# Kernel optimization log

Hardware: AMD Instinct MI355X
Metric: run time of the kernel (lower is better)

The kernel has to match this reference:

```python
import jax, jax.numpy as jnp
import numpy as np

B, N_Q, N_KV, D, H = 2, 2048, 2048, 512, 8
HD = D // H
NEG = -10000.0
LN_EPS = 1e-5


def setup_inputs() -> dict:
    key = jax.random.key(0)
    ks = jax.random.split(key, 8)
    s = 1.0 / np.sqrt(D)
    return {
        "query": jax.random.normal(ks[0], (B, N_Q, D), jnp.float32),
        "key_value": jax.random.normal(ks[1], (B, N_KV, D), jnp.float32),
        "Wq": jax.random.normal(ks[2], (D, D), jnp.float32) * s,
        "bq": jnp.zeros((D,), jnp.float32),
        "Wk": jax.random.normal(ks[3], (D, D), jnp.float32) * s,
        "bk": jnp.zeros((D,), jnp.float32),
        "Wv": jax.random.normal(ks[4], (D, D), jnp.float32) * s,
        "bv": jnp.zeros((D,), jnp.float32),
        "ln_gamma": jnp.ones((D,), jnp.float32),
        "ln_beta": jnp.zeros((D,), jnp.float32),
    }


def reference(query, key_value, Wq, bq, Wk, bk, Wv, bv, ln_gamma, ln_beta):
    # combined sequence [B, S, D], S = N_q + N_kv
    combined = jnp.concatenate([query, key_value], axis=1)
    Bt, S, _ = combined.shape
    n_q = query.shape[1]

    def heads(x, W, b):
        return (x @ W + b).reshape(Bt, S, H, HD)

    q = heads(combined, Wq, bq)  # [B,S,H,hd]
    k = heads(combined, Wk, bk)
    v = heads(combined, Wv, bv)

    scores = jnp.einsum("bqhd,bkhd->bhqk", q, k) / jnp.sqrt(
        jnp.asarray(HD, q.dtype)
    )
    # additive mask: -10000 on key columns < N_q for every query row
    key_mask = jnp.where(jnp.arange(S) < n_q, jnp.asarray(NEG, q.dtype), 0.0)
    probs = jax.nn.softmax(scores + key_mask[None, None, None, :], axis=-1)
    ctx = jnp.einsum("bhqk,bkhd->bqhd", probs, v).reshape(Bt, S, D)

    attended_q = ctx[:, :n_q, :]  # [B, N_q, D]
    resid = query + attended_q  # dropout is identity in eval
    mu = jnp.mean(resid, axis=-1, keepdims=True)
    var = jnp.var(resid, axis=-1, keepdims=True)
    out = (resid - mu) / jnp.sqrt(var + LN_EPS) * ln_gamma + ln_beta
    return out
```

## Files before the change

kernel.cpp:

```cpp
#include <hip/hip_runtime.h>
#include <stdint.h>

#define B_     2
#define NQ     2048
#define NKV    2048
#define D_     512
#define H_     8
#define HD     64
#define MROWS  4096
#define NSPLIT 4
#define SKEYS  (NKV / NSPLIT)

typedef unsigned short u16;
typedef __attribute__((ext_vector_type(4))) unsigned short u16x4;
typedef __attribute__((ext_vector_type(8))) unsigned short u16x8;
typedef __attribute__((ext_vector_type(8))) __bf16 bf16x8;
typedef __attribute__((ext_vector_type(4))) float f32x4;

__device__ __forceinline__ u16 f2bf(float f) {
  union { float f; unsigned int u; } v; v.f = f;
  unsigned int u = v.u;
  unsigned int r = (u + 0x7FFFu + ((u >> 16) & 1u)) >> 16;
  return (u16)r;
}
__device__ __forceinline__ float bf2f(u16 b) {
  union { unsigned int u; float f; } v; v.u = ((unsigned int)b) << 16;
  return v.f;
}
__device__ __forceinline__ unsigned cvtpk(float a, float b) {
  unsigned r;
  asm("v_cvt_pk_bf16_f32 %0, %1, %2" : "=v"(r) : "v"(a), "v"(b));
  return r;
}

__device__ __forceinline__ f32x4 mfma16(u16x8 a, u16x8 b, f32x4 c) {
  return __builtin_amdgcn_mfma_f32_16x16x32_bf16(
      __builtin_bit_cast(bf16x8, a), __builtin_bit_cast(bf16x8, b), c, 0, 0, 0);
}

#define QSCL 0.18033688011112042f

__global__ __launch_bounds__(256) void cast_act_kernel(
    const float* __restrict__ q, const float* __restrict__ kv,
    u16* __restrict__ qb, u16* __restrict__ kvb) {
  int i = blockIdx.x * 256 + threadIdx.x;
  float4 a = ((const float4*)q)[i];
  float4 b = ((const float4*)kv)[i];
  u16x4 ua = { f2bf(a.x), f2bf(a.y), f2bf(a.z), f2bf(a.w) };
  u16x4 ub = { f2bf(b.x), f2bf(b.y), f2bf(b.z), f2bf(b.w) };
  ((u16x4*)qb)[i]  = ua;
  ((u16x4*)kvb)[i] = ub;
}

__global__ __launch_bounds__(256) void wtrans_kernel(
    const float* __restrict__ Wq, const float* __restrict__ Wk,
    const float* __restrict__ Wv,
    u16* __restrict__ wqt, u16* __restrict__ wkt, u16* __restrict__ wvt) {
  __shared__ float tile[32][33];
  int bx = blockIdx.x;
  int which = bx >> 8;
  int t = bx & 255;
  int tr = t >> 4, tc = t & 15;
  const float* W = (which == 0) ? Wq : (which == 1) ? Wk : Wv;
  u16* WT = (which == 0) ? wqt : (which == 1) ? wkt : wvt;

  int tx = threadIdx.x & 31, ty = threadIdx.x >> 5;
#pragma unroll
  for (int i = 0; i < 4; ++i)
    tile[ty + 8 * i][tx] = W[(size_t)(tr * 32 + ty + 8 * i) * D_ + tc * 32 + tx];
  __syncthreads();
#pragma unroll
  for (int i = 0; i < 4; ++i)
    WT[(size_t)(tc * 32 + ty + 8 * i) * D_ + tr * 32 + tx] =
        f2bf(tile[tx][ty + 8 * i]);
}

__global__ __launch_bounds__(256, 3) void gemm_qkv(
    const u16* __restrict__ qb, const u16* __restrict__ kvb,
    const u16* __restrict__ wqt, const u16* __restrict__ wkt,
    const u16* __restrict__ wvt,
    const float* __restrict__ bq, const float* __restrict__ bk,
    const float* __restrict__ bv,
    u16* __restrict__ Qp, u16* __restrict__ Kp, u16* __restrict__ VpT) {
  int lane = threadIdx.x & 63, w = threadIdx.x >> 6;
  int wr = w >> 1, wc = w & 1;
  int cl = lane & 15, g = lane >> 4;
  int cb = blockIdx.y;
  int which = cb >> 2;
  int row0 = blockIdx.x * 64, col0 = (cb & 3) * 128;

  const u16* A   = (which == 0) ? qb : kvb;
  const u16* WT  = (which == 0) ? wqt : (which == 1) ? wkt : wvt;
  const float* bias = (which == 0) ? bq : (which == 1) ? bk : bv;
  u16* Out = (which == 0) ? Qp : (which == 1) ? Kp : VpT;
  float oscale = (which == 0) ? QSCL : 1.0f;

  f32x4 acc[2][4] = {};
  const u16* Abase = A  + (size_t)(row0 + wr * 32 + cl) * D_ + g * 8;
  const u16* Bbase = WT + (size_t)(col0 + wc * 64 + cl) * D_ + g * 8;

  u16x8 afA[2], bfA[4], afB[2], bfB[4];
#pragma unroll
  for (int i = 0; i < 2; ++i) afA[i] = *(const u16x8*)(Abase + (size_t)i * 16 * D_);
#pragma unroll
  for (int j = 0; j < 4; ++j) bfA[j] = *(const u16x8*)(Bbase + (size_t)j * 16 * D_);

#pragma unroll
  for (int kk = 0; kk < 16; ++kk) {
    const u16x8* ca = (kk & 1) ? afB : afA;
    const u16x8* cw = (kk & 1) ? bfB : bfA;
    u16x8* na = (kk & 1) ? afA : afB;
    u16x8* nw = (kk & 1) ? bfA : bfB;
    if (kk < 15) {
      int k0 = kk * 32 + 32;
#pragma unroll
      for (int i = 0; i < 2; ++i) na[i] = *(const u16x8*)(Abase + (size_t)i * 16 * D_ + k0);
#pragma unroll
      for (int j = 0; j < 4; ++j) nw[j] = *(const u16x8*)(Bbase + (size_t)j * 16 * D_ + k0);
    }
#pragma unroll
    for (int i = 0; i < 2; ++i)
#pragma unroll
      for (int j = 0; j < 4; ++j)
        acc[i][j] = mfma16(ca[i], cw[j], acc[i][j]);
  }

#pragma unroll
  for (int j = 0; j < 4; ++j) {
    int col = col0 + wc * 64 + j * 16 + cl;
    float bv2 = bias[col];
#pragma unroll
    for (int i = 0; i < 2; ++i) {
      int rowb = row0 + wr * 32 + i * 16 + g * 4;
      if (which != 2) {
#pragma unroll
        for (int r = 0; r < 4; ++r)
          Out[(size_t)(rowb + r) * D_ + col] = f2bf((acc[i][j][r] + bv2) * oscale);
      } else {
        int b_ = rowb >> 11, key = rowb & (NKV - 1);
        u16x4 pk = { f2bf(acc[i][j][0] + bv2), f2bf(acc[i][j][1] + bv2),
                     f2bf(acc[i][j][2] + bv2), f2bf(acc[i][j][3] + bv2) };
        *(u16x4*)(Out + (size_t)b_ * (D_ * NKV) + (size_t)col * NKV + key) = pk;
      }
    }
  }
}

__global__ __launch_bounds__(64, 2) void attn_kernel(
    const u16* __restrict__ Q, const u16* __restrict__ K,
    const u16* __restrict__ VpT, u16* __restrict__ opart,
    float* __restrict__ ml) {
  __shared__ union __align__(16) {
    u16 p[64][66];
    unsigned t[64][33];
  } sm;

  int lane = threadIdx.x;
  int cl = lane & 15, g = lane >> 4;
  int q0 = blockIdx.x * 64;
  int s  = blockIdx.y;
  int bh = blockIdx.z;
  int b = bh >> 3, h = bh & 7;

  u16x8 qf[4][2];
  {
    const u16* Qb = Q + ((size_t)(b * NQ + q0 + cl)) * D_ + h * HD + g * 8;
#pragma unroll
    for (int f = 0; f < 4; ++f)
#pragma unroll
      for (int kk = 0; kk < 2; ++kk)
        qf[f][kk] = *(const u16x8*)(Qb + (size_t)f * 16 * D_ + kk * 32);
  }

  const u16* kptr[4];
  const u16* vptr[4];
#pragma unroll
  for (int kf_ = 0; kf_ < 4; ++kf_)
    kptr[kf_] = K + ((size_t)b * NKV + s * SKEYS + kf_ * 16 + cl) * D_ + h * HD + g * 8;
#pragma unroll
  for (int j = 0; j < 4; ++j)
    vptr[j] = VpT + (size_t)b * (D_ * NKV) + (size_t)(h * HD + j * 16 + cl) * NKV
                  + s * SKEYS + g * 8;

  f32x4 o[4][4] = {};
  float lsum[4] = { 0.f, 0.f, 0.f, 0.f };

  const int NT = SKEYS / 64;

  for (int t = 0; t < NT; ++t) {
    u16x8 kf[4][2];
#pragma unroll
    for (int kf_ = 0; kf_ < 4; ++kf_)
#pragma unroll
      for (int kk = 0; kk < 2; ++kk)
        kf[kf_][kk] = *(const u16x8*)(kptr[kf_] + kk * 32);

    f32x4 sa[4][4] = {};
    __builtin_amdgcn_s_setprio(1);
#pragma unroll
    for (int kk = 0; kk < 2; ++kk)
#pragma unroll
      for (int kf_ = 0; kf_ < 4; ++kf_)
#pragma unroll
        for (int f = 0; f < 4; ++f)
          sa[kf_][f] = mfma16(kf[kf_][kk], qf[f][kk], sa[kf_][f]);
    __builtin_amdgcn_s_setprio(0);

    u16x8 vf[4][2];
#pragma unroll
    for (int j = 0; j < 4; ++j)
#pragma unroll
      for (int kk = 0; kk < 2; ++kk)
        vf[j][kk] = *(const u16x8*)(vptr[j] + kk * 32);

#pragma unroll
    for (int f = 0; f < 4; ++f) {
      float ps = 0.f;
#pragma unroll
      for (int kf_ = 0; kf_ < 4; ++kf_)
#pragma unroll
        for (int r = 0; r < 4; ++r) {
          float p = exp2f(sa[kf_][f][r]);
          sa[kf_][f][r] = p;
          ps += p;
        }
      lsum[f] += ps;
    }

#pragma unroll
    for (int f = 0; f < 4; ++f)
#pragma unroll
      for (int kf_ = 0; kf_ < 4; ++kf_) {
        unsigned lo = cvtpk(sa[kf_][f][0], sa[kf_][f][1]);
        unsigned hi = cvtpk(sa[kf_][f][2], sa[kf_][f][3]);
        unsigned* P32 = (unsigned*)&sm.p[f * 16 + cl][kf_ * 16 + g * 4];
        P32[0] = lo;
        P32[1] = hi;
      }

#pragma unroll
    for (int kk = 0; kk < 2; ++kk) {
      __builtin_amdgcn_s_setprio(1);
#pragma unroll
      for (int f = 0; f < 4; ++f) {
        u16x8 pa = *(const u16x8*)&sm.p[f * 16 + cl][kk * 32 + g * 8];
#pragma unroll
        for (int j = 0; j < 4; ++j)
          o[f][j] = mfma16(vf[j][kk], pa, o[f][j]);
      }
      __builtin_amdgcn_s_setprio(0);
    }

#pragma unroll
    for (int kf_ = 0; kf_ < 4; ++kf_) kptr[kf_] += 64 * D_;
#pragma unroll
    for (int j = 0; j < 4; ++j) vptr[j] += 64;
  }

#pragma unroll
  for (int f = 0; f < 4; ++f) {
    lsum[f] += __shfl_xor(lsum[f], 16, 64);
    lsum[f] += __shfl_xor(lsum[f], 32, 64);
  }

#pragma unroll
  for (int f = 0; f < 4; ++f)
#pragma unroll
    for (int j = 0; j < 4; ++j) {
      int row = f * 16 + cl;
      sm.t[row][j * 8 + g * 2 + 0] = cvtpk(o[f][j][0], o[f][j][1]);
      sm.t[row][j * 8 + g * 2 + 1] = cvtpk(o[f][j][2], o[f][j][3]);
    }
  if (g == 0) {
#pragma unroll
    for (int f = 0; f < 4; ++f) {
      size_t mi = ((size_t)(bh * NSPLIT + s) * NQ + q0 + f * 16 + cl) * 2;
      ml[mi]     = 0.f;
      ml[mi + 1] = lsum[f];
    }
  }
  __syncthreads();
  {
    int row = lane;
    u16* op = opart + (size_t)(bh * NSPLIT + s) * NQ * HD + (size_t)(q0 + row) * HD;
#pragma unroll
    for (int i = 0; i < 8; ++i) {
      uint4 v;
      v.x = sm.t[row][i * 4 + 0];
      v.y = sm.t[row][i * 4 + 1];
      v.z = sm.t[row][i * 4 + 2];
      v.w = sm.t[row][i * 4 + 3];
      *(uint4*)(op + i * 8) = v;
    }
  }
}

__global__ __launch_bounds__(256) void combine_ln_kernel(
    const float* __restrict__ query, const u16* __restrict__ opart,
    const float* __restrict__ ml,
    const float* __restrict__ gamma, const float* __restrict__ beta,
    float* __restrict__ out) {
  int row = blockIdx.x * 4 + (threadIdx.x >> 6);
  int lane = threadIdx.x & 63;
  int b = row >> 11, q = row & (NQ - 1);
  int h = lane >> 3;

  float ms[NSPLIT], ls[NSPLIT];
  float mmax = -1e30f;
#pragma unroll
  for (int s = 0; s < NSPLIT; ++s) {
    size_t mi = ((size_t)((b * H_ + h) * NSPLIT + s) * NQ + q) * 2;
    ms[s] = ml[mi];
    ls[s] = ml[mi + 1];
    mmax = fmaxf(mmax, ms[s]);
  }
  float lt = 0.f;
#pragma unroll
  for (int s = 0; s < NSPLIT; ++s) lt += ls[s] * exp2f(ms[s] - mmax);
  float inv = 1.f / lt;

  size_t base = (size_t)row * D_;
  const float4* q4 = (const float4*)(query + base);
  float4 a0 = q4[lane * 2], a1 = q4[lane * 2 + 1];
  float x[8] = { a0.x, a0.y, a0.z, a0.w, a1.x, a1.y, a1.z, a1.w };

#pragma unroll
  for (int s = 0; s < NSPLIT; ++s) {
    size_t oi = ((size_t)((b * H_ + h) * NSPLIT + s) * NQ + q) * HD + (lane & 7) * 8;
    u16x8 ov = *(const u16x8*)(opart + oi);
    float sc = exp2f(ms[s] - mmax) * inv;
#pragma unroll
    for (int e = 0; e < 8; ++e) x[e] += bf2f(ov[e]) * sc;
  }

  float sum = 0.f, sq = 0.f;
#pragma unroll
  for (int e = 0; e < 8; ++e) { sum += x[e]; sq += x[e] * x[e]; }
#pragma unroll
  for (int d = 1; d < 64; d <<= 1) {
    sum += __shfl_xor(sum, d, 64);
    sq  += __shfl_xor(sq,  d, 64);
  }
  float mean = sum * (1.f / D_);
  float var  = sq * (1.f / D_) - mean * mean;
  float rstd = rsqrtf(var + 1e-5f);

  const float4* g4  = (const float4*)gamma;
  const float4* be4 = (const float4*)beta;
  float4 g0 = g4[lane * 2], g1 = g4[lane * 2 + 1];
  float4 e0 = be4[lane * 2], e1 = be4[lane * 2 + 1];
  float4 o0, o1;
  o0.x = (x[0] - mean) * rstd * g0.x + e0.x;
  o0.y = (x[1] - mean) * rstd * g0.y + e0.y;
  o0.z = (x[2] - mean) * rstd * g0.z + e0.z;
  o0.w = (x[3] - mean) * rstd * g0.w + e0.w;
  o1.x = (x[4] - mean) * rstd * g1.x + e1.x;
  o1.y = (x[5] - mean) * rstd * g1.y + e1.y;
  o1.z = (x[6] - mean) * rstd * g1.z + e1.z;
  o1.w = (x[7] - mean) * rstd * g1.w + e1.w;
  ((float4*)(out + base))[lane * 2]     = o0;
  ((float4*)(out + base))[lane * 2 + 1] = o1;
}

extern "C" void kernel_launch(void* const* d_in, const int* in_sizes, int n_in,
                              void* d_out, int out_size, void* d_ws, size_t ws_size,
                              hipStream_t stream) {
  const float* query     = (const float*)d_in[0];
  const float* key_value = (const float*)d_in[1];
  const float* Wq = (const float*)d_in[2];
  const float* bq = (const float*)d_in[3];
  const float* Wk = (const float*)d_in[4];
  const float* bk = (const float*)d_in[5];
  const float* Wv = (const float*)d_in[6];
  const float* bv = (const float*)d_in[7];
  const float* gamma = (const float*)d_in[8];
  const float* beta  = (const float*)d_in[9];
  float* out = (float*)d_out;

  char* ws = (char*)d_ws;
  u16* Qp    = (u16*)(ws + 0);
  u16* Kp    = (u16*)(ws + 4194304);
  u16* VpT   = (u16*)(ws + 8388608);
  u16* opart = (u16*)(ws + 12582912);
  float* ml  = (float*)(ws + 29360128);
  u16* qb    = (u16*)(ws + 12582912);
  u16* kvb   = (u16*)(ws + 16777216);
  u16* wqt   = (u16*)(ws + 20971520);
  u16* wkt   = (u16*)(ws + 21495808);
  u16* wvt   = (u16*)(ws + 22020096);

  cast_act_kernel<<<2048, 256, 0, stream>>>(query, key_value, qb, kvb);
  wtrans_kernel<<<768, 256, 0, stream>>>(Wq, Wk, Wv, wqt, wkt, wvt);
  dim3 gg(MROWS / 64, 12);
  gemm_qkv<<<gg, 256, 0, stream>>>(qb, kvb, wqt, wkt, wvt, bq, bk, bv,
                                   Qp, Kp, VpT);
  dim3 ga(NQ / 64, NSPLIT, H_ * B_);
  attn_kernel<<<ga, 64, 0, stream>>>(Qp, Kp, VpT, opart, ml);
  combine_ln_kernel<<<MROWS / 4, 256, 0, stream>>>(query, opart, ml, gamma, beta, out);
}
```

Baseline: 94.10 us.

## Fuse cast and weight-transpose kernels; restructure QKV GEMM with LDS-staged stores

Merges the activation cast and weight transpose into one prep kernel to save a launch. The QKV GEMM becomes single-wave 64x64 tiles with a 4x4 MFMA register block, more blocks, and s_setprio around the MFMA bursts. Outputs are staged through shared memory so global stores are coalesced 16-byte rows, including the transposed V layout. The trade is more per-wave register use and less A/B reuse per block versus better store efficiency.

```diff
diff --git a/kernel.cpp b/kernel.cpp
--- a/kernel.cpp
+++ b/kernel.cpp
@@ -40,54 +40,57 @@
 
 #define QSCL 0.18033688011112042f
 
-__global__ __launch_bounds__(256) void cast_act_kernel(
+__global__ __launch_bounds__(256) void prep_kernel(
     const float* __restrict__ q, const float* __restrict__ kv,
-    u16* __restrict__ qb, u16* __restrict__ kvb) {
-  int i = blockIdx.x * 256 + threadIdx.x;
-  float4 a = ((const float4*)q)[i];
-  float4 b = ((const float4*)kv)[i];
-  u16x4 ua = { f2bf(a.x), f2bf(a.y), f2bf(a.z), f2bf(a.w) };
-  u16x4 ub = { f2bf(b.x), f2bf(b.y), f2bf(b.z), f2bf(b.w) };
-  ((u16x4*)qb)[i]  = ua;
-  ((u16x4*)kvb)[i] = ub;
-}
-
-__global__ __launch_bounds__(256) void wtrans_kernel(
     const float* __restrict__ Wq, const float* __restrict__ Wk,
     const float* __restrict__ Wv,
+    u16* __restrict__ qb, u16* __restrict__ kvb,
     u16* __restrict__ wqt, u16* __restrict__ wkt, u16* __restrict__ wvt) {
   __shared__ float tile[32][33];
   int bx = blockIdx.x;
-  int which = bx >> 8;
-  int t = bx & 255;
-  int tr = t >> 4, tc = t & 15;
-  const float* W = (which == 0) ? Wq : (which == 1) ? Wk : Wv;
-  u16* WT = (which == 0) ? wqt : (which == 1) ? wkt : wvt;
-
-  int tx = threadIdx.x & 31, ty = threadIdx.x >> 5;
-#pragma unroll
-  for (int i = 0; i < 4; ++i)
-    tile[ty + 8 * i][tx] = W[(size_t)(tr * 32 + ty + 8 * i) * D_ + tc * 32 + tx];
-  __syncthreads();
-#pragma unroll
-  for (int i = 0; i < 4; ++i)
-    WT[(size_t)(tc * 32 + ty + 8 * i) * D_ + tr * 32 + tx] =
-        f2bf(tile[tx][ty + 8 * i]);
-}
-
-__global__ __launch_bounds__(256, 3) void gemm_qkv(
+  if (bx < 2048) {
+    int i = bx * 256 + threadIdx.x;
+    float4 a = ((const float4*)q)[i];
+    float4 b = ((const float4*)kv)[i];
+    u16x4 ua = { f2bf(a.x), f2bf(a.y), f2bf(a.z), f2bf(a.w) };
+    u16x4 ub = { f2bf(b.x), f2bf(b.y), f2bf(b.z), f2bf(b.w) };
+    ((u16x4*)qb)[i]  = ua;
+    ((u16x4*)kvb)[i] = ub;
+  } else {
+    int t = bx - 2048;
+    int which = t >> 8;
+    t &= 255;
+    int tr = t >> 4, tc = t & 15;
+    const float* W = (which == 0) ? Wq : (which == 1) ? Wk : Wv;
+    u16* WT = (which == 0) ? wqt : (which == 1) ? wkt : wvt;
+
+    int tx = threadIdx.x & 31, ty = threadIdx.x >> 5;
+#pragma unroll
+    for (int i = 0; i < 4; ++i)
+      tile[ty + 8 * i][tx] = W[(size_t)(tr * 32 + ty + 8 * i) * D_ + tc * 32 + tx];
+    __syncthreads();
+#pragma unroll
+    for (int i = 0; i < 4; ++i)
+      WT[(size_t)(tc * 32 + ty + 8 * i) * D_ + tr * 32 + tx] =
+          f2bf(tile[tx][ty + 8 * i]);
+  }
+}
+
+__global__ __launch_bounds__(64) void gemm_qkv(
     const u16* __restrict__ qb, const u16* __restrict__ kvb,
     const u16* __restrict__ wqt, const u16* __restrict__ wkt,
     const u16* __restrict__ wvt,
     const float* __restrict__ bq, const float* __restrict__ bk,
     const float* __restrict__ bv,
     u16* __restrict__ Qp, u16* __restrict__ Kp, u16* __restrict__ VpT) {
-  int lane = threadIdx.x & 63, w = threadIdx.x >> 6;
-  int wr = w >> 1, wc = w & 1;
+  __shared__ __align__(16) u16 tile[64][72];
+
+  int lane = threadIdx.x;
   int cl = lane & 15, g = lane >> 4;
-  int cb = blockIdx.y;
-  int which = cb >> 2;
-  int row0 = blockIdx.x * 64, col0 = (cb & 3) * 128;
+  int y = blockIdx.y;
+  int which = y >> 3;
+  int col0 = (y & 7) * 64;
+  int row0 = blockIdx.x * 64;
 
   const u16* A   = (which == 0) ? qb : kvb;
   const u16* WT  = (which == 0) ? wqt : (which == 1) ? wkt : wvt;
@@ -95,13 +98,13 @@
   u16* Out = (which == 0) ? Qp : (which == 1) ? Kp : VpT;
   float oscale = (which == 0) ? QSCL : 1.0f;
 
-  f32x4 acc[2][4] = {};
-  const u16* Abase = A  + (size_t)(row0 + wr * 32 + cl) * D_ + g * 8;
-  const u16* Bbase = WT + (size_t)(col0 + wc * 64 + cl) * D_ + g * 8;
-
-  u16x8 afA[2], bfA[4], afB[2], bfB[4];
-#pragma unroll
-  for (int i = 0; i < 2; ++i) afA[i] = *(const u16x8*)(Abase + (size_t)i * 16 * D_);
+  const u16* Abase = A  + (size_t)(row0 + cl) * D_ + g * 8;
+  const u16* Bbase = WT + (size_t)(col0 + cl) * D_ + g * 8;
+
+  f32x4 acc[4][4] = {};
+  u16x8 afA[4], bfA[4], afB[4], bfB[4];
+#pragma unroll
+  for (int i = 0; i < 4; ++i) afA[i] = *(const u16x8*)(Abase + (size_t)i * 16 * D_);
 #pragma unroll
   for (int j = 0; j < 4; ++j) bfA[j] = *(const u16x8*)(Bbase + (size_t)j * 16 * D_);
 
@@ -114,35 +117,43 @@
     if (kk < 15) {
       int k0 = kk * 32 + 32;
 #pragma unroll
-      for (int i = 0; i < 2; ++i) na[i] = *(const u16x8*)(Abase + (size_t)i * 16 * D_ + k0);
+      for (int i = 0; i < 4; ++i) na[i] = *(const u16x8*)(Abase + (size_t)i * 16 * D_ + k0);
 #pragma unroll
       for (int j = 0; j < 4; ++j) nw[j] = *(const u16x8*)(Bbase + (size_t)j * 16 * D_ + k0);
     }
-#pragma unroll
-    for (int i = 0; i < 2; ++i)
+    __builtin_amdgcn_s_setprio(1);
+#pragma unroll
+    for (int i = 0; i < 4; ++i)
 #pragma unroll
       for (int j = 0; j < 4; ++j)
         acc[i][j] = mfma16(ca[i], cw[j], acc[i][j]);
+    __builtin_amdgcn_s_setprio(0);
   }
 
 #pragma unroll
   for (int j = 0; j < 4; ++j) {
-    int col = col0 + wc * 64 + j * 16 + cl;
-    float bv2 = bias[col];
-#pragma unroll
-    for (int i = 0; i < 2; ++i) {
-      int rowb = row0 + wr * 32 + i * 16 + g * 4;
-      if (which != 2) {
-#pragma unroll
-        for (int r = 0; r < 4; ++r)
-          Out[(size_t)(rowb + r) * D_ + col] = f2bf((acc[i][j][r] + bv2) * oscale);
-      } else {
-        int b_ = rowb >> 11, key = rowb & (NKV - 1);
-        u16x4 pk = { f2bf(acc[i][j][0] + bv2), f2bf(acc[i][j][1] + bv2),
-                     f2bf(acc[i][j][2] + bv2), f2bf(acc[i][j][3] + bv2) };
-        *(u16x4*)(Out + (size_t)b_ * (D_ * NKV) + (size_t)col * NKV + key) = pk;
+    float bv2 = bias[col0 + j * 16 + cl];
+#pragma unroll
+    for (int i = 0; i < 4; ++i)
+#pragma unroll
+      for (int r = 0; r < 4; ++r) {
+        u16 val = f2bf((acc[i][j][r] + bv2) * oscale);
+        int rr = i * 16 + g * 4 + r, cc = j * 16 + cl;
+        if (which != 2) tile[rr][cc] = val;
+        else            tile[cc][rr] = val;
       }
-    }
+  }
+  u16* dst;
+  if (which != 2) {
+    dst = Out + (size_t)(row0 + lane) * D_ + col0;
+  } else {
+    int b_ = row0 >> 11, key0 = row0 & (NKV - 1);
+    dst = Out + (size_t)b_ * (D_ * NKV) + (size_t)(col0 + lane) * NKV + key0;
+  }
+#pragma unroll
+  for (int c8 = 0; c8 < 8; ++c8) {
+    uint4 v = *(const uint4*)&tile[lane][c8 * 8];
+    *(uint4*)(dst + c8 * 8) = v;
   }
 }
 
@@ -389,11 +400,11 @@
   u16* wkt   = (u16*)(ws + 21495808);
   u16* wvt   = (u16*)(ws + 22020096);
 
-  cast_act_kernel<<<2048, 256, 0, stream>>>(query, key_value, qb, kvb);
-  wtrans_kernel<<<768, 256, 0, stream>>>(Wq, Wk, Wv, wqt, wkt, wvt);
-  dim3 gg(MROWS / 64, 12);
-  gemm_qkv<<<gg, 256, 0, stream>>>(qb, kvb, wqt, wkt, wvt, bq, bk, bv,
-                                   Qp, Kp, VpT);
+  prep_kernel<<<2816, 256, 0, stream>>>(query, key_value, Wq, Wk, Wv,
+                                        qb, kvb, wqt, wkt, wvt);
+  dim3 gg(MROWS / 64, 24);
+  gemm_qkv<<<gg, 64, 0, stream>>>(qb, kvb, wqt, wkt, wvt, bq, bk, bv,
+                                  Qp, Kp, VpT);
   dim3 ga(NQ / 64, NSPLIT, H_ * B_);
   attn_kernel<<<ga, 64, 0, stream>>>(Qp, Kp, VpT, opart, ml);
   combine_ln_kernel<<<MROWS / 4, 256, 0, stream>>>(query, opart, ml, gamma, beta, out);
```

Measured after the change: 85.49 us. -9.1%, faster.
